# Performance work log

Measured on AMD Instinct MI355X. Metric: run time of the kernel, lower is better.

## Reference

```python
import jax, jax.numpy as jnp
import numpy as np
from jax import lax

DN = ('NCDHW', 'OIDHW', 'NCDHW')
BN_EPS = 1e-5  # eval-mode BatchNorm3d with running_mean=0, running_var=1


def conv3d(x, w, b):
    y = lax.conv_general_dilated(x, w, window_strides=(1, 1, 1),
                                 padding=[(1, 1)] * 3, dimension_numbers=DN)
    return y + b[None, :, None, None, None]


def maxpool2(x):
    return lax.reduce_window(x, -jnp.inf, lax.max,
                             (1, 1, 2, 2, 2), (1, 1, 2, 2, 2), 'VALID')


def spline_block(x, cw, cb, knots, sw, w1, w2, g, beta):
    # SplineConv3d: conv -> (BSpline3D blend with SiLU) -> BN(eval) -> maxpool
    y = conv3d(x, cw, cb)                                   # [b,c,d,h,w]
    basis = jnp.maximum(y[..., None] - knots, 0.0) ** 3     # [b,c,d,h,w,k]
    sp = jnp.einsum('bcdhwk,ck->bcdhw', basis, sw)
    out = (w1[None, :, None, None, None] * sp
           + w2[None, :, None, None, None] * (y * jax.nn.sigmoid(y)))
    scale = (g / jnp.sqrt(1.0 + BN_EPS))[None, :, None, None, None]
    return maxpool2(out * scale + beta[None, :, None, None, None])


def setup_inputs() -> dict:
    key = jax.random.key(0)
    ks = iter(jax.random.split(key, 40))
    def nrm(shape, s=1.0):
        return jax.random.normal(next(ks), shape, dtype=jnp.float32) * s
    d = {}
    d['x'] = nrm((2, 1, 64, 64, 64))
    for cin, cout, t in [(1, 32, '1'), (32, 64, '2'), (64, 128, '3')]:
        d[f'c{t}_w'] = nrm((cout, cin, 3, 3, 3), 0.1)
        d[f'c{t}_b'] = nrm((cout,), 0.01)
        d[f'c{t}_knots'] = jnp.linspace(-1.0, 1.0, 10).astype(jnp.float32)
        d[f'c{t}_sw'] = nrm((cout, 10), 0.2)
        d[f'c{t}_w1'] = nrm((cout,), 0.2)
        d[f'c{t}_w2'] = nrm((cout,), 0.2)
        d[f'bn{t}_g'] = 1.0 + nrm((cout,), 0.1)
        d[f'bn{t}_b'] = nrm((cout,), 0.1)
    d['fc1_w'] = nrm((256, 128), 0.05)
    d['fc1_b'] = nrm((256,), 0.01)
    d['fc2_w'] = nrm((2, 256), 0.05)
    d['fc2_b'] = nrm((2,), 0.01)
    return d


def reference(x,
              c1_w, c1_b, c1_knots, c1_sw, c1_w1, c1_w2, bn1_g, bn1_b,
              c2_w, c2_b, c2_knots, c2_sw, c2_w1, c2_w2, bn2_g, bn2_b,
              c3_w, c3_b, c3_knots, c3_sw, c3_w1, c3_w2, bn3_g, bn3_b,
              fc1_w, fc1_b, fc2_w, fc2_b):
    h = spline_block(x, c1_w, c1_b, c1_knots, c1_sw, c1_w1, c1_w2, bn1_g, bn1_b)
    h = spline_block(h, c2_w, c2_b, c2_knots, c2_sw, c2_w1, c2_w2, bn2_g, bn2_b)
    h = spline_block(h, c3_w, c3_b, c3_knots, c3_sw, c3_w1, c3_w2, bn3_g, bn3_b)
    h = h.mean(axis=(2, 3, 4))          # AdaptiveAvgPool3d((1,1,1)) + flatten
    h = jax.nn.relu(h @ fc1_w.T + fc1_b)  # dropout is identity in eval mode
    return h @ fc2_w.T + fc2_b
```

## Files before the change

kernel.cpp:

```cpp
#include <hip/hip_runtime.h>
#include <math.h>


#define GLOBAL_AS __attribute__((address_space(1)))
#define LDS_AS    __attribute__((address_space(3)))

static __device__ __forceinline__ void async_ld16(const float* g, float* l) {
    __builtin_amdgcn_global_load_lds((const GLOBAL_AS void*)g, (LDS_AS void*)l,
                                     16, 0, 0);
}

template <int TPB_, int CIN, int DEPTH, int G, int PDT, int PHT, int PWT>
__global__ __launch_bounds__(TPB_, 2) void spline_block_kernel(
    const float* __restrict__ x,
    const float* __restrict__ cw,
    const float* __restrict__ cb,
    const float* __restrict__ knots,
    const float* __restrict__ sw,
    const float* __restrict__ w1,
    const float* __restrict__ w2,
    const float* __restrict__ g,
    const float* __restrict__ beta,
    const float* __restrict__ zbuf,
    float* __restrict__ out,
    int N, int Cout, int D, int H, int W,
    int ntiles, int nthw, int ntw)
{
    constexpr int ID     = 2 * PDT + 2;
    constexpr int IH     = 2 * PHT + 2;
    constexpr int PITCH  = 24;
    constexpr int ROWS   = ID * IH;
    constexpr int CHUNKS = ROWS * 6;
    constexpr int PHYS   = ROWS * PITCH;
    constexpr int NCH    = (CHUNKS + TPB_ - 1) / TPB_;
    constexpr int BUFS   = (CIN > DEPTH) ? 2 : 1;
    static_assert(CIN % DEPTH == 0, "cin divisible by depth");
    static_assert(NCH <= 32, "mask fits u32");
    static_assert(PDT * PHT * PWT == TPB_, "one thread per pooled voxel");

    __shared__ __align__(16) float tile[BUFS][DEPTH][PHYS];
    __shared__ float  wlds[CIN * G * 28];
    __shared__ float4 stbl[G * 11];

    const int PD = D >> 1, PH = H >> 1, PW = W >> 1;
    const int groups = Cout / G;
    const int tid = threadIdx.x;

    const int bx      = blockIdx.x;
    const int tile_id = bx % ntiles;
    const int t1      = bx / ntiles;
    const int grp     = t1 % groups;
    const int n       = t1 / groups;
    const int c0      = grp * G;

    const int td  = tile_id / nthw;
    const int rem = tile_id % nthw;
    const int th_ = rem / ntw;
    const int tw_ = rem % ntw;

    for (int i = tid; i < CIN * G * 27; i += TPB_) {
        const int t  = i % 27;
        const int cg = i / 27;
        const int gg = cg % G;
        const int ci = cg / G;
        wlds[cg * 28 + t] = cw[((c0 + gg) * CIN + ci) * 27 + t];
    }
    for (int i = tid; i < G * 11; i += TPB_) {
        const int gg  = i / 11;
        const int cnt = i % 11;
        const int c   = c0 + gg;
        float A = 0.f, B3 = 0.f, C3 = 0.f, Dd = 0.f;
        for (int j = 0; j < cnt; j++) {
            const float s = sw[c * 10 + j];
            const float k = knots[j];
            A  += s;
            B3 += 3.0f * s * k;
            C3 += 3.0f * s * k * k;
            Dd += s * k * k * k;
        }
        stbl[i] = make_float4(A, B3, C3, Dd);
    }

    const int pwl = tid % PWT;
    const int phl = (tid / PWT) % PHT;
    const int pdl = tid / (PWT * PHT);

    const int pd0 = td * PDT, ph0 = th_ * PHT, pw0 = tw_ * PWT;
    const int d0 = 2 * pd0 - 1, h0 = 2 * ph0 - 1;
    const int w0 = 2 * pw0 - 1;
    const int wb = w0 & ~3;
    const int woff = w0 - wb;

    int off[NCH];
    unsigned vm = 0;
#pragma unroll
    for (int k = 0; k < NCH; k++) {
        const int chunk = tid + TPB_ * k;
        const int row = chunk / 6, cs = chunk - row * 6;
        const int dz = row / IH, hy = row - dz * IH;
        const int dd = d0 + dz, hh = h0 + hy;
        const int wsd = wb + cs * 4;
        const bool ok = (chunk < CHUNKS) &
                        ((unsigned)dd < (unsigned)D) &
                        ((unsigned)hh < (unsigned)H) &
                        ((unsigned)wsd < (unsigned)W);
        off[k] = ok ? (dd * H + hh) * W + wsd : 0;
        vm |= (unsigned)ok << k;
    }

    const size_t chstride = (size_t)D * H * W;
    const float* xn = x + (size_t)n * CIN * chstride;

    float acc[G][8];
#pragma unroll
    for (int gg = 0; gg < G; gg++) {
        const float bias = cb[c0 + gg];
#pragma unroll
        for (int i = 0; i < 8; i++) acc[gg][i] = bias;
    }

    __syncthreads();

#pragma unroll 1
    for (int s = 0; s < DEPTH && s < CIN; s++) {
        const float* xc = xn + (size_t)s * chstride;
        float* dst = &tile[0][s][0];
#pragma unroll
        for (int k = 0; k < NCH; k++) {
            const int chunk = tid + TPB_ * k;
            if ((k + 1) * TPB_ <= CHUNKS || chunk < CHUNKS) {
                const float* src = ((vm >> k) & 1) ? (xc + off[k]) : zbuf;
                async_ld16(src, dst + chunk * 4);
            }
        }
    }
    __syncthreads();

    int cur = 0;
#pragma unroll 1
    for (int base = 0; base < CIN; base += DEPTH) {
        if (base + DEPTH < CIN) {
#pragma unroll 1
            for (int s = 0; s < DEPTH; s++) {
                const float* xc = xn + (size_t)(base + DEPTH + s) * chstride;
                float* dst = &tile[cur ^ (BUFS - 1)][s][0];
#pragma unroll
                for (int k = 0; k < NCH; k++) {
                    const int chunk = tid + TPB_ * k;
                    if ((k + 1) * TPB_ <= CHUNKS || chunk < CHUNKS) {
                        const float* src = ((vm >> k) & 1) ? (xc + off[k]) : zbuf;
                        async_ld16(src, dst + chunk * 4);
                    }
                }
            }
        }

#pragma unroll 1
        for (int s = 0; s < DEPTH; s++) {
            const int ci = base + s;
            const float* tb = &tile[cur][s][0];
            float r[64];
#pragma unroll
            for (int dz = 0; dz < 4; dz++)
#pragma unroll
            for (int dy = 0; dy < 4; dy++) {
                const int rb = ((2 * pdl + dz) * IH + (2 * phl + dy)) * PITCH +
                               woff + 2 * pwl;
                r[(dz * 4 + dy) * 4 + 0] = tb[rb + 0];
                r[(dz * 4 + dy) * 4 + 1] = tb[rb + 1];
                r[(dz * 4 + dy) * 4 + 2] = tb[rb + 2];
                r[(dz * 4 + dy) * 4 + 3] = tb[rb + 3];
            }

#pragma unroll
            for (int gg = 0; gg < G; gg++) {
                const float4* w4p = (const float4*)&wlds[(ci * G + gg) * 28];
#pragma unroll
                for (int ch = 0; ch < 7; ch++) {
                    const float4 wv = w4p[ch];
#pragma unroll
                    for (int j = 0; j < 4; j++) {
                        const int tap = ch * 4 + j;
                        if (tap < 27) {
                            const float wvj = (j == 0) ? wv.x : (j == 1) ? wv.y
                                            : (j == 2) ? wv.z : wv.w;
                            const int kd = tap / 9, kh = (tap % 9) / 3, kw = tap % 3;
#pragma unroll
                            for (int od = 0; od < 2; od++)
#pragma unroll
                            for (int oh = 0; oh < 2; oh++)
#pragma unroll
                            for (int ow = 0; ow < 2; ow++)
                                acc[gg][(od * 2 + oh) * 2 + ow] =
                                    fmaf(wvj,
                                         r[((od + kd) * 4 + (oh + kh)) * 4 + (ow + kw)],
                                         acc[gg][(od * 2 + oh) * 2 + ow]);
                        }
                    }
                }
            }
        }

        if (base + DEPTH < CIN) {
            __syncthreads();
            cur ^= 1;
        }
    }

    const int pdg = pd0 + pdl, phg = ph0 + phl, pwg = pw0 + pwl;
#pragma unroll
    for (int gg = 0; gg < G; gg++) {
        const int c = c0 + gg;
        const float W1 = w1[c], W2 = w2[c];
        const float scale = g[c] * rsqrtf(1.0f + 1e-5f);
        const float bb = beta[c];

        float m = -INFINITY;
#pragma unroll
        for (int i = 0; i < 8; i++) {
            const float y = acc[gg][i];
            int idx = (int)floorf((y + 1.0f) * 4.5f) + 1;
            idx = min(max(idx, 0), 10);
            const float4 cf = stbl[gg * 11 + idx];
            const float sp = ((cf.x * y - cf.y) * y + cf.z) * y - cf.w;
            const float silu = y / (1.0f + __expf(-y));
            const float o = fmaf(W1 * sp + W2 * silu, scale, bb);
            m = fmaxf(m, o);
        }
        out[((size_t)(n * Cout + c) * PD + pdg) * PH * PW + phg * PW + pwg] = m;
    }
}

__global__ __launch_bounds__(64) void mean_kernel(
    const float* __restrict__ h, float* __restrict__ out, int S)
{
    const int nc = blockIdx.x;
    const int lane = threadIdx.x;
    const float* p = h + (size_t)nc * S;
    float s = 0.0f;
    for (int i = lane; i < S; i += 64) s += p[i];
#pragma unroll
    for (int off = 32; off > 0; off >>= 1) s += __shfl_down(s, off, 64);
    if (lane == 0) out[nc] = s / (float)S;
}

__global__ __launch_bounds__(256) void fc_kernel(
    const float* __restrict__ pooled,
    const float* __restrict__ w1, const float* __restrict__ b1,
    const float* __restrict__ w2, const float* __restrict__ b2,
    float* __restrict__ out)
{
    __shared__ float hbuf[2][256];
    const int j = threadIdx.x;
#pragma unroll
    for (int nn = 0; nn < 2; nn++) {
        float s = b1[j];
        for (int k = 0; k < 128; k++)
            s = fmaf(pooled[nn * 128 + k], w1[j * 128 + k], s);
        hbuf[nn][j] = fmaxf(s, 0.0f);
    }
    __syncthreads();
    const int wid = j >> 6, lane = j & 63;
    const int nn = wid >> 1, oo = wid & 1;
    float s = 0.0f;
    for (int k = lane; k < 256; k += 64) s += hbuf[nn][k] * w2[oo * 256 + k];
#pragma unroll
    for (int off = 32; off > 0; off >>= 1) s += __shfl_down(s, off, 64);
    if (lane == 0) out[nn * 2 + oo] = s + b2[oo];
}

extern "C" void kernel_launch(void* const* d_in, const int* in_sizes, int n_in,
                              void* d_out, int out_size, void* d_ws, size_t ws_size,
                              hipStream_t stream) {
    const float* x      = (const float*)d_in[0];
    const float* c1_w   = (const float*)d_in[1];
    const float* c1_b   = (const float*)d_in[2];
    const float* c1_kn  = (const float*)d_in[3];
    const float* c1_sw  = (const float*)d_in[4];
    const float* c1_w1  = (const float*)d_in[5];
    const float* c1_w2  = (const float*)d_in[6];
    const float* bn1_g  = (const float*)d_in[7];
    const float* bn1_b  = (const float*)d_in[8];
    const float* c2_w   = (const float*)d_in[9];
    const float* c2_b   = (const float*)d_in[10];
    const float* c2_kn  = (const float*)d_in[11];
    const float* c2_sw  = (const float*)d_in[12];
    const float* c2_w1  = (const float*)d_in[13];
    const float* c2_w2  = (const float*)d_in[14];
    const float* bn2_g  = (const float*)d_in[15];
    const float* bn2_b  = (const float*)d_in[16];
    const float* c3_w   = (const float*)d_in[17];
    const float* c3_b   = (const float*)d_in[18];
    const float* c3_kn  = (const float*)d_in[19];
    const float* c3_sw  = (const float*)d_in[20];
    const float* c3_w1  = (const float*)d_in[21];
    const float* c3_w2  = (const float*)d_in[22];
    const float* bn3_g  = (const float*)d_in[23];
    const float* bn3_b  = (const float*)d_in[24];
    const float* fc1_w  = (const float*)d_in[25];
    const float* fc1_b  = (const float*)d_in[26];
    const float* fc2_w  = (const float*)d_in[27];
    const float* fc2_b  = (const float*)d_in[28];

    float* ws = (float*)d_ws;
    float* h1     = ws;
    float* h2     = h1 + 2097152;
    float* h3     = h2 + 524288;
    float* pooled = h3 + 131072;
    float* zbuf   = pooled + 256;

    hipMemsetAsync(zbuf, 0, 64, stream);

    spline_block_kernel<256, 1, 1, 4, 4, 8, 8><<<dim3(2048), dim3(256), 0, stream>>>(
        x, c1_w, c1_b, c1_kn, c1_sw, c1_w1, c1_w2, bn1_g, bn1_b, zbuf, h1,
        2, 32, 64, 64, 64, 128, 16, 4);
    spline_block_kernel<256, 32, 1, 4, 4, 8, 8><<<dim3(512), dim3(256), 0, stream>>>(
        h1, c2_w, c2_b, c2_kn, c2_sw, c2_w1, c2_w2, bn2_g, bn2_b, zbuf, h2,
        2, 64, 32, 32, 32, 16, 4, 2);
    spline_block_kernel<128, 64, 4, 4, 2, 8, 8><<<dim3(256), dim3(128), 0, stream>>>(
        h2, c3_w, c3_b, c3_kn, c3_sw, c3_w1, c3_w2, bn3_g, bn3_b, zbuf, h3,
        2, 128, 16, 16, 16, 4, 1, 1);
    mean_kernel<<<dim3(256), dim3(64), 0, stream>>>(h3, pooled, 512);
    fc_kernel<<<dim3(1), dim3(256), 0, stream>>>(pooled, fc1_w, fc1_b, fc2_w, fc2_b,
                                                 (float*)d_out);
}
```

Baseline: 386.2 us.

## Split input channels across thread groups with LDS reduction for layer-3 conv

Replaces the multi-channel staging depth parameter with a split-K scheme. The block is divided into CSPLIT groups, each accumulating the convolution over its own slice of input channels into its own double-buffered tile. Partial sums are then reduced through LDS scratch, and group 0 applies the bias and the spline/BN/pool epilogue. Layer 3 now uses 4-way channel splitting, a smaller spatial tile and 512 blocks of 256 threads, which adds parallelism to the small last layer at the cost of an extra reduction and idle threads during the epilogue.

```diff
diff --git a/kernel.cpp b/kernel.cpp
--- a/kernel.cpp
+++ b/kernel.cpp
@@ -10,7 +10,7 @@
                                      16, 0, 0);
 }
 
-template <int TPB_, int CIN, int DEPTH, int G, int PDT, int PHT, int PWT>
+template <int TPB_, int CIN, int CSPLIT, int G, int PDT, int PHT, int PWT>
 __global__ __launch_bounds__(TPB_, 2) void spline_block_kernel(
     const float* __restrict__ x,
     const float* __restrict__ cw,
@@ -26,25 +26,32 @@
     int N, int Cout, int D, int H, int W,
     int ntiles, int nthw, int ntw)
 {
+    constexpr int SP     = PDT * PHT * PWT;
+    constexpr int CPG    = CIN / CSPLIT;
     constexpr int ID     = 2 * PDT + 2;
     constexpr int IH     = 2 * PHT + 2;
     constexpr int PITCH  = 24;
     constexpr int ROWS   = ID * IH;
     constexpr int CHUNKS = ROWS * 6;
     constexpr int PHYS   = ROWS * PITCH;
-    constexpr int NCH    = (CHUNKS + TPB_ - 1) / TPB_;
-    constexpr int BUFS   = (CIN > DEPTH) ? 2 : 1;
-    static_assert(CIN % DEPTH == 0, "cin divisible by depth");
+    constexpr int NCH    = (CHUNKS + SP - 1) / SP;
+    constexpr int BUFS   = (CPG > 1) ? 2 : 1;
+    static_assert(SP * CSPLIT == TPB_, "block = CSPLIT x SP");
+    static_assert(CIN % CSPLIT == 0, "cin divisible");
     static_assert(NCH <= 32, "mask fits u32");
-    static_assert(PDT * PHT * PWT == TPB_, "one thread per pooled voxel");
-
-    __shared__ __align__(16) float tile[BUFS][DEPTH][PHYS];
+    static_assert(CSPLIT == 1 ||
+                  (CSPLIT - 1) * SP * G * 8 <= CSPLIT * BUFS * PHYS,
+                  "reduction scratch fits in tile");
+
+    __shared__ __align__(16) float tile[CSPLIT][BUFS][PHYS];
     __shared__ float  wlds[CIN * G * 28];
     __shared__ float4 stbl[G * 11];
 
     const int PD = D >> 1, PH = H >> 1, PW = W >> 1;
     const int groups = Cout / G;
-    const int tid = threadIdx.x;
+    const int tid  = threadIdx.x;
+    const int cg   = tid / SP;
+    const int stid = tid % SP;
 
     const int bx      = blockIdx.x;
     const int tile_id = bx % ntiles;
@@ -52,6 +59,7 @@
     const int grp     = t1 % groups;
     const int n       = t1 / groups;
     const int c0      = grp * G;
+    const int cinbase = cg * CPG;
 
     const int td  = tile_id / nthw;
     const int rem = tile_id % nthw;
@@ -60,10 +68,10 @@
 
     for (int i = tid; i < CIN * G * 27; i += TPB_) {
         const int t  = i % 27;
-        const int cg = i / 27;
-        const int gg = cg % G;
-        const int ci = cg / G;
-        wlds[cg * 28 + t] = cw[((c0 + gg) * CIN + ci) * 27 + t];
+        const int cgr = i / 27;
+        const int gg = cgr % G;
+        const int ci = cgr / G;
+        wlds[cgr * 28 + t] = cw[((c0 + gg) * CIN + ci) * 27 + t];
     }
     for (int i = tid; i < G * 11; i += TPB_) {
         const int gg  = i / 11;
@@ -81,9 +89,9 @@
         stbl[i] = make_float4(A, B3, C3, Dd);
     }
 
-    const int pwl = tid % PWT;
-    const int phl = (tid / PWT) % PHT;
-    const int pdl = tid / (PWT * PHT);
+    const int pwl = stid % PWT;
+    const int phl = (stid / PWT) % PHT;
+    const int pdl = stid / (PWT * PHT);
 
     const int pd0 = td * PDT, ph0 = th_ * PHT, pw0 = tw_ * PWT;
     const int d0 = 2 * pd0 - 1, h0 = 2 * ph0 - 1;
@@ -95,7 +103,7 @@
     unsigned vm = 0;
 #pragma unroll
     for (int k = 0; k < NCH; k++) {
-        const int chunk = tid + TPB_ * k;
+        const int chunk = stid + SP * k;
         const int row = chunk / 6, cs = chunk - row * 6;
         const int dz = row / IH, hy = row - dz * IH;
         const int dd = d0 + dz, hh = h0 + hy;
@@ -113,22 +121,19 @@
 
     float acc[G][8];
 #pragma unroll
-    for (int gg = 0; gg < G; gg++) {
-        const float bias = cb[c0 + gg];
-#pragma unroll
-        for (int i = 0; i < 8; i++) acc[gg][i] = bias;
-    }
+    for (int gg = 0; gg < G; gg++)
+#pragma unroll
+        for (int i = 0; i < 8; i++) acc[gg][i] = 0.0f;
 
     __syncthreads();
 
-#pragma unroll 1
-    for (int s = 0; s < DEPTH && s < CIN; s++) {
-        const float* xc = xn + (size_t)s * chstride;
-        float* dst = &tile[0][s][0];
+    {
+        const float* xc = xn + (size_t)cinbase * chstride;
+        float* dst = &tile[cg][0][0];
 #pragma unroll
         for (int k = 0; k < NCH; k++) {
-            const int chunk = tid + TPB_ * k;
-            if ((k + 1) * TPB_ <= CHUNKS || chunk < CHUNKS) {
+            const int chunk = stid + SP * k;
+            if ((k + 1) * SP <= CHUNKS || chunk < CHUNKS) {
                 const float* src = ((vm >> k) & 1) ? (xc + off[k]) : zbuf;
                 async_ld16(src, dst + chunk * 4);
             }
@@ -138,96 +143,114 @@
 
     int cur = 0;
 #pragma unroll 1
-    for (int base = 0; base < CIN; base += DEPTH) {
-        if (base + DEPTH < CIN) {
-#pragma unroll 1
-            for (int s = 0; s < DEPTH; s++) {
-                const float* xc = xn + (size_t)(base + DEPTH + s) * chstride;
-                float* dst = &tile[cur ^ (BUFS - 1)][s][0];
-#pragma unroll
-                for (int k = 0; k < NCH; k++) {
-                    const int chunk = tid + TPB_ * k;
-                    if ((k + 1) * TPB_ <= CHUNKS || chunk < CHUNKS) {
-                        const float* src = ((vm >> k) & 1) ? (xc + off[k]) : zbuf;
-                        async_ld16(src, dst + chunk * 4);
+    for (int s = 0; s < CPG; s++) {
+        if (s + 1 < CPG) {
+            const float* xc = xn + (size_t)(cinbase + s + 1) * chstride;
+            float* dst = &tile[cg][cur ^ (BUFS - 1)][0];
+#pragma unroll
+            for (int k = 0; k < NCH; k++) {
+                const int chunk = stid + SP * k;
+                if ((k + 1) * SP <= CHUNKS || chunk < CHUNKS) {
+                    const float* src = ((vm >> k) & 1) ? (xc + off[k]) : zbuf;
+                    async_ld16(src, dst + chunk * 4);
+                }
+            }
+        }
+
+        const int ci = cinbase + s;
+        const float* tb = &tile[cg][cur][0];
+        float r[64];
+#pragma unroll
+        for (int dz = 0; dz < 4; dz++)
+#pragma unroll
+        for (int dy = 0; dy < 4; dy++) {
+            const int rb = ((2 * pdl + dz) * IH + (2 * phl + dy)) * PITCH +
+                           woff + 2 * pwl;
+            r[(dz * 4 + dy) * 4 + 0] = tb[rb + 0];
+            r[(dz * 4 + dy) * 4 + 1] = tb[rb + 1];
+            r[(dz * 4 + dy) * 4 + 2] = tb[rb + 2];
+            r[(dz * 4 + dy) * 4 + 3] = tb[rb + 3];
+        }
+
+#pragma unroll
+        for (int gg = 0; gg < G; gg++) {
+            const float4* w4p = (const float4*)&wlds[(ci * G + gg) * 28];
+#pragma unroll
+            for (int ch = 0; ch < 7; ch++) {
+                const float4 wv = w4p[ch];
+#pragma unroll
+                for (int j = 0; j < 4; j++) {
+                    const int tap = ch * 4 + j;
+                    if (tap < 27) {
+                        const float wvj = (j == 0) ? wv.x : (j == 1) ? wv.y
+                                        : (j == 2) ? wv.z : wv.w;
+                        const int kd = tap / 9, kh = (tap % 9) / 3, kw = tap % 3;
+#pragma unroll
+                        for (int od = 0; od < 2; od++)
+#pragma unroll
+                        for (int oh = 0; oh < 2; oh++)
+#pragma unroll
+                        for (int ow = 0; ow < 2; ow++)
+                            acc[gg][(od * 2 + oh) * 2 + ow] =
+                                fmaf(wvj,
+                                     r[((od + kd) * 4 + (oh + kh)) * 4 + (ow + kw)],
+                                     acc[gg][(od * 2 + oh) * 2 + ow]);
                     }
                 }
             }
         }
 
-#pragma unroll 1
-        for (int s = 0; s < DEPTH; s++) {
-            const int ci = base + s;
-            const float* tb = &tile[cur][s][0];
-            float r[64];
-#pragma unroll
-            for (int dz = 0; dz < 4; dz++)
-#pragma unroll
-            for (int dy = 0; dy < 4; dy++) {
-                const int rb = ((2 * pdl + dz) * IH + (2 * phl + dy)) * PITCH +
-                               woff + 2 * pwl;
-                r[(dz * 4 + dy) * 4 + 0] = tb[rb + 0];
-                r[(dz * 4 + dy) * 4 + 1] = tb[rb + 1];
-                r[(dz * 4 + dy) * 4 + 2] = tb[rb + 2];
-                r[(dz * 4 + dy) * 4 + 3] = tb[rb + 3];
-            }
-
-#pragma unroll
-            for (int gg = 0; gg < G; gg++) {
-                const float4* w4p = (const float4*)&wlds[(ci * G + gg) * 28];
-#pragma unroll
-                for (int ch = 0; ch < 7; ch++) {
-                    const float4 wv = w4p[ch];
-#pragma unroll
-                    for (int j = 0; j < 4; j++) {
-                        const int tap = ch * 4 + j;
-                        if (tap < 27) {
-                            const float wvj = (j == 0) ? wv.x : (j == 1) ? wv.y
-                                            : (j == 2) ? wv.z : wv.w;
-                            const int kd = tap / 9, kh = (tap % 9) / 3, kw = tap % 3;
-#pragma unroll
-                            for (int od = 0; od < 2; od++)
-#pragma unroll
-                            for (int oh = 0; oh < 2; oh++)
-#pragma unroll
-                            for (int ow = 0; ow < 2; ow++)
-                                acc[gg][(od * 2 + oh) * 2 + ow] =
-                                    fmaf(wvj,
-                                         r[((od + kd) * 4 + (oh + kh)) * 4 + (ow + kw)],
-                                         acc[gg][(od * 2 + oh) * 2 + ow]);
-                        }
-                    }
-                }
-            }
-        }
-
-        if (base + DEPTH < CIN) {
+        if (s + 1 < CPG) {
             __syncthreads();
             cur ^= 1;
         }
     }
 
-    const int pdg = pd0 + pdl, phg = ph0 + phl, pwg = pw0 + pwl;
-#pragma unroll
-    for (int gg = 0; gg < G; gg++) {
-        const int c = c0 + gg;
-        const float W1 = w1[c], W2 = w2[c];
-        const float scale = g[c] * rsqrtf(1.0f + 1e-5f);
-        const float bb = beta[c];
-
-        float m = -INFINITY;
-#pragma unroll
-        for (int i = 0; i < 8; i++) {
-            const float y = acc[gg][i];
-            int idx = (int)floorf((y + 1.0f) * 4.5f) + 1;
-            idx = min(max(idx, 0), 10);
-            const float4 cf = stbl[gg * 11 + idx];
-            const float sp = ((cf.x * y - cf.y) * y + cf.z) * y - cf.w;
-            const float silu = y / (1.0f + __expf(-y));
-            const float o = fmaf(W1 * sp + W2 * silu, scale, bb);
-            m = fmaxf(m, o);
-        }
-        out[((size_t)(n * Cout + c) * PD + pdg) * PH * PW + phg * PW + pwg] = m;
+    float* af = &acc[0][0];
+    if (CSPLIT > 1) {
+        __syncthreads();
+        float* scratch = &tile[0][0][0];
+        if (cg > 0) {
+#pragma unroll
+            for (int idx = 0; idx < G * 8; idx++)
+                scratch[(idx * (CSPLIT - 1) + (cg - 1)) * SP + stid] = af[idx];
+        }
+        __syncthreads();
+        if (cg == 0) {
+#pragma unroll
+            for (int idx = 0; idx < G * 8; idx++) {
+                float s = af[idx];
+                for (int j = 0; j < CSPLIT - 1; j++)
+                    s += scratch[(idx * (CSPLIT - 1) + j) * SP + stid];
+                af[idx] = s;
+            }
+        }
+    }
+
+    if (cg == 0) {
+        const int pdg = pd0 + pdl, phg = ph0 + phl, pwg = pw0 + pwl;
+#pragma unroll
+        for (int gg = 0; gg < G; gg++) {
+            const int c = c0 + gg;
+            const float bias = cb[c];
+            const float W1 = w1[c], W2 = w2[c];
+            const float scale = g[c] * rsqrtf(1.0f + 1e-5f);
+            const float bb = beta[c];
+
+            float m = -INFINITY;
+#pragma unroll
+            for (int i = 0; i < 8; i++) {
+                const float y = acc[gg][i] + bias;
+                int idx = (int)floorf((y + 1.0f) * 4.5f) + 1;
+                idx = min(max(idx, 0), 10);
+                const float4 cf = stbl[gg * 11 + idx];
+                const float sp = ((cf.x * y - cf.y) * y + cf.z) * y - cf.w;
+                const float silu = y / (1.0f + __expf(-y));
+                const float o = fmaf(W1 * sp + W2 * silu, scale, bb);
+                m = fmaxf(m, o);
+            }
+            out[((size_t)(n * Cout + c) * PD + pdg) * PH * PW + phg * PW + pwg] = m;
+        }
     }
 }
 
@@ -317,9 +340,9 @@
     spline_block_kernel<256, 32, 1, 4, 4, 8, 8><<<dim3(512), dim3(256), 0, stream>>>(
         h1, c2_w, c2_b, c2_kn, c2_sw, c2_w1, c2_w2, bn2_g, bn2_b, zbuf, h2,
         2, 64, 32, 32, 32, 16, 4, 2);
-    spline_block_kernel<128, 64, 4, 4, 2, 8, 8><<<dim3(256), dim3(128), 0, stream>>>(
+    spline_block_kernel<256, 64, 4, 4, 2, 4, 8><<<dim3(512), dim3(256), 0, stream>>>(
         h2, c3_w, c3_b, c3_kn, c3_sw, c3_w1, c3_w2, bn3_g, bn3_b, zbuf, h3,
-        2, 128, 16, 16, 16, 4, 1, 1);
+        2, 128, 16, 16, 16, 8, 2, 1);
     mean_kernel<<<dim3(256), dim3(64), 0, stream>>>(h3, pooled, 512);
     fc_kernel<<<dim3(1), dim3(256), 0, stream>>>(pooled, fc1_w, fc1_b, fc2_w, fc2_b,
                                                  (float*)d_out);
```

After: 338.1 us. -12.5%, faster.
